# Kernel optimization log

Measured on AMD Instinct MI355X. Metric: run time of the kernel, lower is better.

## Reference

```python
import jax, jax.numpy as jnp
import numpy as np

B, N, H, OUT, T = 8192, 82, 10, 5, 3  # batch, n_nodes, hidden, output_channel, time_step


def setup_inputs() -> dict:
    key = jax.random.key(0)
    ks = jax.random.split(key, 20)

    def lin(kw, kb, fin, fout):
        w = jax.random.normal(kw, (fout, fin), jnp.float32) * (1.0 / np.sqrt(fin))
        b = jax.random.normal(kb, (fout,), jnp.float32) * 0.01
        return w, b

    w3w, b3w = lin(ks[0], ks[1], 2 * H, H)
    w3u, b3u = lin(ks[2], ks[3], H, H)
    w4w, b4w = lin(ks[4], ks[5], 2 * H, H)
    w5w, b5w = lin(ks[6], ks[7], 2 * H, H)
    w5u, b5u = lin(ks[8], ks[9], H, H)
    wout, bout = lin(ks[10], ks[11], 2 * H, OUT)
    return {
        'x': jax.random.normal(ks[12], (B, N, H), jnp.float32),
        'in_adj': jax.random.uniform(ks[13], (N, N), jnp.float32),
        'out_adj': jax.random.uniform(ks[14], (N, N), jnp.float32),
        'w3w': w3w, 'b3w': b3w, 'w3u': w3u, 'b3u': b3u,
        'w4w': w4w, 'b4w': b4w, 'w5w': w5w, 'b5w': b5w,
        'w5u': w5u, 'b5u': b5u, 'wout': wout, 'bout': bout,
    }


def _dense(v, w, b):
    return v @ w.T + b


def reference(x, in_adj, out_adj, w3w, b3w, w3u, b3u, w4w, b4w,
              w5w, b5w, w5u, b5u, wout, bout):
    b, n, h = x.shape
    nodes = x  # [B, N, H]
    fn = nodes.reshape(b * n, h)
    for _ in range(T):
        # neighbor aggregation; adjacency shared across batch (torch tiles it with repeat)
        a_in = jnp.einsum('ij,bjh->bih', in_adj, nodes)
        a_out = jnp.einsum('ij,bjh->bih', out_adj, nodes)
        av = jnp.concatenate([a_in, a_out], axis=-1).reshape(b * n, 2 * h)
        fn = nodes.reshape(b * n, h)
        zv = jax.nn.sigmoid(_dense(av, w3w, b3w) + _dense(fn, w3u, b3u))
        # NOTE: original torch code (bug) reuses fc_eq3_u here instead of fc_eq4_u
        rv = jax.nn.sigmoid(_dense(av, w4w, b4w) + _dense(fn, w3u, b3u))
        hv = jnp.tanh(_dense(av, w5w, b5w) + _dense(rv * fn, w5u, b5u))
        fn = (1.0 - zv) * fn + zv * hv
        nodes = fn.reshape(b, n, h)
    out_in = jnp.concatenate([fn, x.reshape(b * n, h)], axis=1)
    output = jnp.tanh(_dense(out_in, wout, bout))
    return output, fn
```

## Files before the change

### kernel.cpp

```cpp
#include <hip/hip_runtime.h>
#include <hip/hip_bf16.h>
#include <math.h>

#define B_TOTAL 8192
#define NN      82
#define HH      10
#define OUTC    5
#define TSTEP   3
#define NB      2
#define THREADS 256
#define KP      96
#define RS      10
#define NROWS   26
#define XS      104
#define UTSF    164

#define XTL_OFF 5408
#define WS_OFF  13120
#define SMEM_BYTES 16960

#define W3W 0
#define W4W 200
#define W5W 400
#define W3U 600
#define W5U 700
#define WOUT 800
#define B3W 900
#define B4W 910
#define B5W 920
#define B3U 930
#define B5U 940
#define BOUT 950

typedef __bf16 bf16x8 __attribute__((ext_vector_type(8)));
typedef float  f32x4  __attribute__((ext_vector_type(4)));
typedef float  f32x2  __attribute__((ext_vector_type(2)));

__device__ __forceinline__ float sigmoid_(float x) {
    return 1.0f / (1.0f + __expf(-x));
}
__device__ __forceinline__ float tanh_(float x) {
    float e = __expf(2.0f * x);
    return 1.0f - 2.0f / (e + 1.0f);
}
__device__ __forceinline__ f32x2 ld2(const float* p) {
    return *reinterpret_cast<const f32x2*>(p);
}
__device__ __forceinline__ f32x2 fma2(f32x2 a, f32x2 b, f32x2 c) {
    return __builtin_elementwise_fma(a, b, c);
}

__global__ void prep_adj_kernel(const float* __restrict__ in_adj,
                                const float* __restrict__ out_adj,
                                __hip_bfloat16* __restrict__ adjP) {
    int idx = blockIdx.x * blockDim.x + threadIdx.x;
    if (idx < 2 * KP * KP) {
        int a   = idx / (KP * KP);
        int rem = idx - a * (KP * KP);
        int i = rem / KP;
        int j = rem - i * KP;
        float v = 0.0f;
        if (i < NN && j < NN) v = (a == 0) ? in_adj[i * NN + j] : out_adj[i * NN + j];
        __hip_bfloat16 hi = __float2bfloat16(v);
        __hip_bfloat16 lo = __float2bfloat16(v - __bfloat162float(hi));
        adjP[idx]               = hi;
        adjP[2 * KP * KP + idx] = lo;
    }
}

extern "C" __global__ __launch_bounds__(THREADS, 5)
void ggnn_kernel(const float* __restrict__ x,
                 const __hip_bfloat16* __restrict__ adjP,
                 const float* __restrict__ w3w, const float* __restrict__ b3w,
                 const float* __restrict__ w3u, const float* __restrict__ b3u,
                 const float* __restrict__ w4w, const float* __restrict__ b4w,
                 const float* __restrict__ w5w, const float* __restrict__ b5w,
                 const float* __restrict__ w5u, const float* __restrict__ b5u,
                 const float* __restrict__ wout, const float* __restrict__ bout,
                 float* __restrict__ out0, float* __restrict__ out_fn)
{
    __shared__ __align__(16) unsigned char smem[SMEM_BYTES];
    __hip_bfloat16* XtH = reinterpret_cast<__hip_bfloat16*>(smem);
    __hip_bfloat16* XtL = reinterpret_cast<__hip_bfloat16*>(smem + XTL_OFF);
    float* uT = reinterpret_cast<float*>(smem);
    float* wS = reinterpret_cast<float*>(smem + WS_OFF);

    const int t     = threadIdx.x;
    const int bbase = blockIdx.x * NB;
    const int bl    = t / NN;
    const int node  = t - bl * NN;
    const bool act  = (bl < NB) && (bbase + bl < B_TOTAL);
    const int b     = bbase + bl;

    const int lane = t & 63;
    const int w    = t >> 6;
    const int lo16 = lane & 15;
    const int quad = lane >> 4;

    for (int i = t; i < 200; i += THREADS) {
        wS[W3W + i] = w3w[i];
        wS[W4W + i] = w4w[i];
        wS[W5W + i] = w5w[i];
    }
    if (t < 100) {
        wS[W3U + t]  = w3u[t];
        wS[W5U + t]  = w5u[t];
        wS[WOUT + t] = wout[t];
    }
    if (t < 10) {
        wS[B3W + t] = b3w[t];
        wS[B4W + t] = b4w[t];
        wS[B5W + t] = b5w[t];
        wS[B3U + t] = b3u[t];
        wS[B5U + t] = b5u[t];
    }
    if (t < OUTC) wS[BOUT + t] = bout[t];

    int ntile_c[3], adj_c[3], Boff[3];
    #pragma unroll
    for (int c = 0; c < 3; ++c) {
        int co = w * 3 + c;
        int nt = co >> 1;
        int ad = co & 1;
        ntile_c[c] = nt;
        adj_c[c]   = ad;
        Boff[c] = ad * KP * KP + (nt * 16 + lo16) * KP + quad * 8;
    }

    for (int idx = t; idx < NB * NN * HH; idx += THREADS) {
        int b_l = idx / (NN * HH);
        int rem = idx - b_l * (NN * HH);
        int j   = rem / HH;
        int h   = rem - j * HH;
        size_t g = (size_t)bbase * NN * HH + idx;
        float v = (g < (size_t)B_TOTAL * NN * HH) ? x[g] : 0.0f;
        __hip_bfloat16 hi = __float2bfloat16(v);
        __hip_bfloat16 lo = __float2bfloat16(v - __bfloat162float(hi));
        XtH[(b_l * RS + h) * XS + j] = hi;
        XtL[(b_l * RS + h) * XS + j] = lo;
    }
    {
        __hip_bfloat16 z = __float2bfloat16(0.0f);
        for (int idx = t; idx < 2 * (NB * RS) * (KP - NN); idx += THREADS) {
            int a   = idx / ((NB * RS) * (KP - NN));
            int rem = idx - a * ((NB * RS) * (KP - NN));
            int r   = rem / (KP - NN);
            int c   = rem - r * (KP - NN);
            (a ? XtL : XtH)[r * XS + NN + c] = z;
        }
    }

    f32x2 fn2[5];
    if (act) {
        const float* xr = x + ((size_t)b * NN + node) * HH;
        #pragma unroll
        for (int p = 0; p < 5; ++p) {
            float2 v = reinterpret_cast<const float2*>(xr)[p];
            fn2[p].x = v.x; fn2[p].y = v.y;
        }
    }

    #pragma unroll 1
    for (int step = 0; step < TSTEP; ++step) {
        __syncthreads();

        f32x4 acc[NB][3];
        #pragma unroll
        for (int m = 0; m < NB; ++m)
            #pragma unroll
            for (int c = 0; c < 3; ++c) acc[m][c] = (f32x4){0, 0, 0, 0};

        #pragma unroll 1
        for (int k = 0; k < 3; ++k) {
            bf16x8 ah[NB], al[NB];
            #pragma unroll
            for (int m = 0; m < NB; ++m) {
                ah[m] = *reinterpret_cast<const bf16x8*>(&XtH[(m * RS + lo16) * XS + quad * 8 + k * 32]);
                al[m] = *reinterpret_cast<const bf16x8*>(&XtL[(m * RS + lo16) * XS + quad * 8 + k * 32]);
            }
            #pragma unroll
            for (int c = 0; c < 3; ++c) {
                const __hip_bfloat16* bp = adjP + Boff[c] + k * 32;
                bf16x8 bh  = *reinterpret_cast<const bf16x8*>(bp);
                bf16x8 bl_ = *reinterpret_cast<const bf16x8*>(bp + 2 * KP * KP);
                #pragma unroll
                for (int m = 0; m < NB; ++m) {
                    acc[m][c] = __builtin_amdgcn_mfma_f32_16x16x32_bf16(ah[m], bh,  acc[m][c], 0, 0, 0);
                    acc[m][c] = __builtin_amdgcn_mfma_f32_16x16x32_bf16(al[m], bh,  acc[m][c], 0, 0, 0);
                    acc[m][c] = __builtin_amdgcn_mfma_f32_16x16x32_bf16(ah[m], bl_, acc[m][c], 0, 0, 0);
                }
            }
        }

        __syncthreads();

        #pragma unroll
        for (int m = 0; m < NB; ++m) {
            #pragma unroll
            for (int c = 0; c < 3; ++c) {
                int i = ntile_c[c] * 16 + lo16;
                if (i < NN) {
                    int col = m * NN + i;
                    float* plane0 = uT + (adj_c[c] ? 10 * UTSF : 0);
                    if (quad < 2) {
                        #pragma unroll
                        for (int r = 0; r < 4; ++r)
                            plane0[(quad * 4 + r) * UTSF + col] = acc[m][c][r];
                    } else if (quad == 2) {
                        plane0[8 * UTSF + col] = acc[m][c][0];
                        plane0[9 * UTSF + col] = acc[m][c][1];
                    }
                }
            }
        }

        __syncthreads();

        f32x2 av2[10];
        if (act) {
            #pragma unroll
            for (int p = 0; p < 5; ++p) {
                av2[p].x     = uT[(2 * p) * UTSF + t];
                av2[p].y     = uT[(2 * p + 1) * UTSF + t];
                av2[5 + p].x = uT[(10 + 2 * p) * UTSF + t];
                av2[5 + p].y = uT[(10 + 2 * p + 1) * UTSF + t];
            }
        }

        __syncthreads();

        if (act) {
            float zv[HH];
            f32x2 rf2[5];
            #pragma unroll
            for (int h = 0; h < HH; ++h) {
                f32x2 su = {0.0f, 0.0f};
                #pragma unroll
                for (int p = 0; p < 5; ++p)
                    su = fma2(ld2(&wS[W3U + h * HH + 2 * p]), fn2[p], su);
                float u3h = wS[B3U + h] + su.x + su.y;

                f32x2 z2 = {0.0f, 0.0f}, r2 = {0.0f, 0.0f};
                #pragma unroll
                for (int p = 0; p < 10; ++p) {
                    z2 = fma2(ld2(&wS[W3W + h * 20 + 2 * p]), av2[p], z2);
                    r2 = fma2(ld2(&wS[W4W + h * 20 + 2 * p]), av2[p], r2);
                }
                zv[h] = sigmoid_(wS[B3W + h] + z2.x + z2.y + u3h);
                float rv = sigmoid_(wS[B4W + h] + r2.x + r2.y + u3h);
                float fnh = (h & 1) ? fn2[h >> 1].y : fn2[h >> 1].x;
                if (h & 1) rf2[h >> 1].y = rv * fnh; else rf2[h >> 1].x = rv * fnh;
            }

            #pragma unroll
            for (int h = 0; h < HH; ++h) {
                f32x2 s2 = {0.0f, 0.0f};
                #pragma unroll
                for (int p = 0; p < 10; ++p)
                    s2 = fma2(ld2(&wS[W5W + h * 20 + 2 * p]), av2[p], s2);
                #pragma unroll
                for (int p = 0; p < 5; ++p)
                    s2 = fma2(ld2(&wS[W5U + h * HH + 2 * p]), rf2[p], s2);
                float hv = tanh_(wS[B5W + h] + wS[B5U + h] + s2.x + s2.y);
                float fnh = (h & 1) ? fn2[h >> 1].y : fn2[h >> 1].x;
                fnh = fnh + zv[h] * (hv - fnh);
                if (h & 1) fn2[h >> 1].y = fnh; else fn2[h >> 1].x = fnh;
            }

            if (step < TSTEP - 1) {
                #pragma unroll
                for (int h = 0; h < HH; ++h) {
                    float fnh = (h & 1) ? fn2[h >> 1].y : fn2[h >> 1].x;
                    __hip_bfloat16 hi = __float2bfloat16(fnh);
                    __hip_bfloat16 lo = __float2bfloat16(fnh - __bfloat162float(hi));
                    XtH[(bl * RS + h) * XS + node] = hi;
                    XtL[(bl * RS + h) * XS + node] = lo;
                }
            }
        }
        if (step < TSTEP - 1) {
            __hip_bfloat16 z = __float2bfloat16(0.0f);
            for (int idx = t; idx < 2 * (NB * RS) * (KP - NN); idx += THREADS) {
                int a   = idx / ((NB * RS) * (KP - NN));
                int rem = idx - a * ((NB * RS) * (KP - NN));
                int r   = rem / (KP - NN);
                int c   = rem - r * (KP - NN);
                (a ? XtL : XtH)[r * XS + NN + c] = z;
            }
        }
    }

    if (act) {
        size_t row = (size_t)b * NN + node;
        const float* xr = x + row * HH;
        f32x2 xi2[5];
        #pragma unroll
        for (int p = 0; p < 5; ++p) {
            float2 v = reinterpret_cast<const float2*>(xr)[p];
            xi2[p].x = v.x; xi2[p].y = v.y;
        }

        #pragma unroll
        for (int c = 0; c < OUTC; ++c) {
            f32x2 s2 = {0.0f, 0.0f};
            #pragma unroll
            for (int p = 0; p < 5; ++p) {
                s2 = fma2(ld2(&wS[WOUT + c * 20 + 2 * p]),      fn2[p], s2);
                s2 = fma2(ld2(&wS[WOUT + c * 20 + 10 + 2 * p]), xi2[p], s2);
            }
            out0[row * OUTC + c] = tanh_(wS[BOUT + c] + s2.x + s2.y);
        }
        #pragma unroll
        for (int p = 0; p < 5; ++p) {
            reinterpret_cast<float2*>(out_fn + row * HH)[p] =
                make_float2(fn2[p].x, fn2[p].y);
        }
    }
}

extern "C" void kernel_launch(void* const* d_in, const int* in_sizes, int n_in,
                              void* d_out, int out_size, void* d_ws, size_t ws_size,
                              hipStream_t stream) {
    const float* x       = (const float*)d_in[0];
    const float* in_adj  = (const float*)d_in[1];
    const float* out_adj = (const float*)d_in[2];
    const float* w3w = (const float*)d_in[3];
    const float* b3w = (const float*)d_in[4];
    const float* w3u = (const float*)d_in[5];
    const float* b3u = (const float*)d_in[6];
    const float* w4w = (const float*)d_in[7];
    const float* b4w = (const float*)d_in[8];
    const float* w5w = (const float*)d_in[9];
    const float* b5w = (const float*)d_in[10];
    const float* w5u = (const float*)d_in[11];
    const float* b5u = (const float*)d_in[12];
    const float* wout = (const float*)d_in[13];
    const float* bout = (const float*)d_in[14];

    __hip_bfloat16* adjP = (__hip_bfloat16*)d_ws;
    float* out0   = (float*)d_out;
    float* out_fn = out0 + (size_t)B_TOTAL * NN * OUTC;

    prep_adj_kernel<<<(2 * KP * KP + 255) / 256, 256, 0, stream>>>(in_adj, out_adj, adjP);

    int grid = (B_TOTAL + NB - 1) / NB;
    ggnn_kernel<<<grid, THREADS, 0, stream>>>(
        x, adjP, w3w, b3w, w3u, b3u, w4w, b4w, w5w, b5w, w5u, b5u,
        wout, bout, out0, out_fn);
}
```

Measured before the change: 254.2 us.

## Process three batches per block with fp16 aggregation buffer and separate smem regions

Raises batches per block from two to three (246 active threads of 256) and loops over batch m-tiles sequentially, using fewer accumulator registers. The aggregation output buffer moves to its own shared-memory region stored as fp16 pairs. This removes the aliasing with the X tiles, drops two barriers per step, and lets the padding be zeroed once at start instead of every step. The trade-offs are fp16 rounding of aggregated values, larger shared memory that may cut occupancy, and serialized MFMA tiles.

After: 285.7 us. 12.4% more time.

```diff
diff --git a/kernel.cpp b/kernel.cpp
--- a/kernel.cpp
+++ b/kernel.cpp
@@ -1,5 +1,6 @@
 #include <hip/hip_runtime.h>
 #include <hip/hip_bf16.h>
+#include <hip/hip_fp16.h>
 #include <math.h>
 
 #define B_TOTAL 8192
@@ -7,17 +8,18 @@
 #define HH      10
 #define OUTC    5
 #define TSTEP   3
-#define NB      2
+#define NB      3
 #define THREADS 256
 #define KP      96
 #define RS      10
-#define NROWS   26
+#define NROWS   36
 #define XS      104
-#define UTSF    164
-
-#define XTL_OFF 5408
-#define WS_OFF  13120
-#define SMEM_BYTES 16960
+#define UTS     248
+
+#define XTL_OFF 7488
+#define UT_OFF  14976
+#define WS_OFF  24896
+#define SMEM_BYTES 28736
 
 #define W3W 0
 #define W4W 200
@@ -82,8 +84,8 @@
     __shared__ __align__(16) unsigned char smem[SMEM_BYTES];
     __hip_bfloat16* XtH = reinterpret_cast<__hip_bfloat16*>(smem);
     __hip_bfloat16* XtL = reinterpret_cast<__hip_bfloat16*>(smem + XTL_OFF);
-    float* uT = reinterpret_cast<float*>(smem);
-    float* wS = reinterpret_cast<float*>(smem + WS_OFF);
+    __half*         uH  = reinterpret_cast<__half*>(smem + UT_OFF);
+    float*          wS  = reinterpret_cast<float*>(smem + WS_OFF);
 
     const int t     = threadIdx.x;
     const int bbase = blockIdx.x * NB;
@@ -97,6 +99,9 @@
     const int lo16 = lane & 15;
     const int quad = lane >> 4;
 
+    for (int i = t; i < UT_OFF / 16; i += THREADS)
+        reinterpret_cast<f32x4*>(smem)[i] = (f32x4){0, 0, 0, 0};
+
     for (int i = t; i < 200; i += THREADS) {
         wS[W3W + i] = w3w[i];
         wS[W4W + i] = w4w[i];
@@ -115,6 +120,8 @@
         wS[B5U + t] = b5u[t];
     }
     if (t < OUTC) wS[BOUT + t] = bout[t];
+
+    __syncthreads();
 
     int ntile_c[3], adj_c[3], Boff[3];
     #pragma unroll
@@ -139,16 +146,6 @@
         XtH[(b_l * RS + h) * XS + j] = hi;
         XtL[(b_l * RS + h) * XS + j] = lo;
     }
-    {
-        __hip_bfloat16 z = __float2bfloat16(0.0f);
-        for (int idx = t; idx < 2 * (NB * RS) * (KP - NN); idx += THREADS) {
-            int a   = idx / ((NB * RS) * (KP - NN));
-            int rem = idx - a * ((NB * RS) * (KP - NN));
-            int r   = rem / (KP - NN);
-            int c   = rem - r * (KP - NN);
-            (a ? XtL : XtH)[r * XS + NN + c] = z;
-        }
-    }
 
     f32x2 fn2[5];
     if (act) {
@@ -164,51 +161,38 @@
     for (int step = 0; step < TSTEP; ++step) {
         __syncthreads();
 
-        f32x4 acc[NB][3];
-        #pragma unroll
-        for (int m = 0; m < NB; ++m)
-            #pragma unroll
-            for (int c = 0; c < 3; ++c) acc[m][c] = (f32x4){0, 0, 0, 0};
-
         #pragma unroll 1
-        for (int k = 0; k < 3; ++k) {
-            bf16x8 ah[NB], al[NB];
-            #pragma unroll
-            for (int m = 0; m < NB; ++m) {
-                ah[m] = *reinterpret_cast<const bf16x8*>(&XtH[(m * RS + lo16) * XS + quad * 8 + k * 32]);
-                al[m] = *reinterpret_cast<const bf16x8*>(&XtL[(m * RS + lo16) * XS + quad * 8 + k * 32]);
-            }
-            #pragma unroll
-            for (int c = 0; c < 3; ++c) {
-                const __hip_bfloat16* bp = adjP + Boff[c] + k * 32;
-                bf16x8 bh  = *reinterpret_cast<const bf16x8*>(bp);
-                bf16x8 bl_ = *reinterpret_cast<const bf16x8*>(bp + 2 * KP * KP);
-                #pragma unroll
-                for (int m = 0; m < NB; ++m) {
-                    acc[m][c] = __builtin_amdgcn_mfma_f32_16x16x32_bf16(ah[m], bh,  acc[m][c], 0, 0, 0);
-                    acc[m][c] = __builtin_amdgcn_mfma_f32_16x16x32_bf16(al[m], bh,  acc[m][c], 0, 0, 0);
-                    acc[m][c] = __builtin_amdgcn_mfma_f32_16x16x32_bf16(ah[m], bl_, acc[m][c], 0, 0, 0);
+        for (int mtile = 0; mtile < NB; ++mtile) {
+            f32x4 acc[3] = {{0,0,0,0}, {0,0,0,0}, {0,0,0,0}};
+            #pragma unroll 1
+            for (int k = 0; k < 3; ++k) {
+                bf16x8 ah = *reinterpret_cast<const bf16x8*>(&XtH[(mtile * RS + lo16) * XS + quad * 8 + k * 32]);
+                bf16x8 al = *reinterpret_cast<const bf16x8*>(&XtL[(mtile * RS + lo16) * XS + quad * 8 + k * 32]);
+                #pragma unroll
+                for (int c = 0; c < 3; ++c) {
+                    const __hip_bfloat16* bp = adjP + Boff[c] + k * 32;
+                    bf16x8 bh  = *reinterpret_cast<const bf16x8*>(bp);
+                    bf16x8 bl_ = *reinterpret_cast<const bf16x8*>(bp + 2 * KP * KP);
+                    acc[c] = __builtin_amdgcn_mfma_f32_16x16x32_bf16(ah, bh,  acc[c], 0, 0, 0);
+                    acc[c] = __builtin_amdgcn_mfma_f32_16x16x32_bf16(al, bh,  acc[c], 0, 0, 0);
+                    acc[c] = __builtin_amdgcn_mfma_f32_16x16x32_bf16(ah, bl_, acc[c], 0, 0, 0);
                 }
             }
-        }
-
-        __syncthreads();
-
-        #pragma unroll
-        for (int m = 0; m < NB; ++m) {
             #pragma unroll
             for (int c = 0; c < 3; ++c) {
                 int i = ntile_c[c] * 16 + lo16;
                 if (i < NN) {
-                    int col = m * NN + i;
-                    float* plane0 = uT + (adj_c[c] ? 10 * UTSF : 0);
+                    int col   = mtile * NN + i;
+                    int pbase = adj_c[c] * 5;
                     if (quad < 2) {
                         #pragma unroll
-                        for (int r = 0; r < 4; ++r)
-                            plane0[(quad * 4 + r) * UTSF + col] = acc[m][c][r];
+                        for (int r = 0; r < 4; ++r) {
+                            int h = quad * 4 + r;
+                            uH[((pbase + (h >> 1)) * UTS + col) * 2 + (h & 1)] = __float2half(acc[c][r]);
+                        }
                     } else if (quad == 2) {
-                        plane0[8 * UTSF + col] = acc[m][c][0];
-                        plane0[9 * UTSF + col] = acc[m][c][1];
+                        uH[((pbase + 4) * UTS + col) * 2 + 0] = __float2half(acc[c][0]);
+                        uH[((pbase + 4) * UTS + col) * 2 + 1] = __float2half(acc[c][1]);
                     }
                 }
             }
@@ -216,20 +200,18 @@
 
         __syncthreads();
 
-        f32x2 av2[10];
         if (act) {
+            f32x2 av2[10];
             #pragma unroll
             for (int p = 0; p < 5; ++p) {
-                av2[p].x     = uT[(2 * p) * UTSF + t];
-                av2[p].y     = uT[(2 * p + 1) * UTSF + t];
-                av2[5 + p].x = uT[(10 + 2 * p) * UTSF + t];
-                av2[5 + p].y = uT[(10 + 2 * p + 1) * UTSF + t];
-            }
-        }
-
-        __syncthreads();
-
-        if (act) {
+                __half2 hin  = *reinterpret_cast<const __half2*>(uH + (p * UTS + t) * 2);
+                __half2 hout = *reinterpret_cast<const __half2*>(uH + ((5 + p) * UTS + t) * 2);
+                float2 fi = __half22float2(hin);
+                float2 fo = __half22float2(hout);
+                av2[p].x = fi.x;     av2[p].y = fi.y;
+                av2[5 + p].x = fo.x; av2[5 + p].y = fo.y;
+            }
+
             float zv[HH];
             f32x2 rf2[5];
             #pragma unroll
@@ -276,16 +258,6 @@
                     XtH[(bl * RS + h) * XS + node] = hi;
                     XtL[(bl * RS + h) * XS + node] = lo;
                 }
-            }
-        }
-        if (step < TSTEP - 1) {
-            __hip_bfloat16 z = __float2bfloat16(0.0f);
-            for (int idx = t; idx < 2 * (NB * RS) * (KP - NN); idx += THREADS) {
-                int a   = idx / ((NB * RS) * (KP - NN));
-                int rem = idx - a * ((NB * RS) * (KP - NN));
-                int r   = rem / (KP - NN);
-                int c   = rem - r * (KP - NN);
-                (a ? XtL : XtH)[r * XS + NN + c] = z;
             }
         }
     }
```
